# Optimization experiments

Hardware: AMD Instinct MI355X
Metric: run time of the kernel (lower is better)

## Reference

```python
import jax, jax.numpy as jnp
import numpy as np

N, E = 100000, 1600000
NFEAT, NHID, NCLASS = 128, 128, 40


def _glorot(key, shape):
    lim = float(np.sqrt(6.0 / (shape[0] + shape[1])))
    return jax.random.uniform(key, shape, jnp.float32, -lim, lim)


def setup_inputs() -> dict:
    key = jax.random.key(0)
    ks = jax.random.split(key, 9)
    x = jax.random.normal(ks[0], (N, NFEAT), jnp.float32)
    edge_index = jax.random.randint(ks[1], (2, E), 0, N, jnp.int32)
    return {
        "x": x,
        "edge_index": edge_index,
        # layer 1: lin_l (aggregated, with bias) and lin_r (root, no bias)
        "W1l": _glorot(ks[2], (NFEAT, NHID)), "b1": jnp.zeros((NHID,), jnp.float32),
        "W1r": _glorot(ks[3], (NFEAT, NHID)),
        "W2l": _glorot(ks[4], (NHID, NHID)), "b2": jnp.zeros((NHID,), jnp.float32),
        "W2r": _glorot(ks[5], (NHID, NHID)),
        "W3l": _glorot(ks[6], (NHID, NCLASS)), "b3": jnp.zeros((NCLASS,), jnp.float32),
        "W3r": _glorot(ks[7], (NHID, NCLASS)),
    }


def _sage_conv(x, src, dst, Wl, bl, Wr):
    # mean-aggregate source features at destination nodes (PyG SAGEConv, aggr='mean')
    msg = x[src]                                                  # [E, d] gather
    agg = jax.ops.segment_sum(msg, dst, num_segments=N)           # [N, d] scatter-add
    deg = jax.ops.segment_sum(jnp.ones((src.shape[0], 1), x.dtype), dst, num_segments=N)
    mean = agg / jnp.maximum(deg, 1.0)
    return mean @ Wl + bl + x @ Wr


def reference(x, edge_index, W1l, b1, W1r, W2l, b2, W2r, W3l, b3, W3r):
    src, dst = edge_index[0], edge_index[1]
    h = jax.nn.relu(_sage_conv(x, src, dst, W1l, b1, W1r))
    # dropout is identity in eval mode (training=False)
    h = jax.nn.relu(_sage_conv(h, src, dst, W2l, b2, W2r))
    embeddings = h
    logits = _sage_conv(h, src, dst, W3l, b3, W3r)
    return jax.nn.log_softmax(logits, axis=1), embeddings
```

## Files before the change

### kernel.cpp

```cpp
#include <hip/hip_runtime.h>
#include <math.h>

#define NCLASS 40
#define BEDG 1024
#define CAP 24576

typedef float f32x4 __attribute__((ext_vector_type(4)));
typedef __bf16 bf16x8 __attribute__((ext_vector_type(8)));

typedef __attribute__((address_space(1))) const void gv_t;
typedef __attribute__((address_space(3))) void lv_t;
#define GLOAD_LDS16(g, l) __builtin_amdgcn_global_load_lds((gv_t*)(g), (lv_t*)(l), 16, 0, 0)
#define NTL(p) __builtin_nontemporal_load(p)

__device__ inline unsigned short f2bf(float f) {
  unsigned u = __float_as_uint(f);
  unsigned r = (u + 0x7fff + ((u >> 16) & 1)) >> 16;
  return (unsigned short)r;
}
__device__ inline float bflo(unsigned v) { return __uint_as_float(v << 16); }
__device__ inline float bfhi(unsigned v) { return __uint_as_float(v & 0xffff0000u); }


__global__ void k_bcount(const int* __restrict__ dst, int E, int PART,
                         int* __restrict__ bcnt) {
  __shared__ int lc[8];
  int k = blockIdx.x;
  if (threadIdx.x < 8) lc[threadIdx.x] = 0;
  __syncthreads();
  int lo = k * BEDG, hi = min(lo + BEDG, E);
  for (int i = lo + threadIdx.x; i < hi; i += blockDim.x)
    atomicAdd(&lc[NTL(&dst[i]) / PART], 1);
  __syncthreads();
  if (threadIdx.x < 8) bcnt[k * 8 + threadIdx.x] = lc[threadIdx.x];
}

__global__ void k_bscanA(int* __restrict__ bcnt, int nbB, int* __restrict__ btot) {
  __shared__ int tmp[256];
  __shared__ int carryS;
  int b = blockIdx.x;
  int tid = threadIdx.x;
  if (tid == 0) carryS = 0;
  __syncthreads();
  for (int c0 = 0; c0 < nbB; c0 += 256) {
    int idx = c0 + tid;
    int v = (idx < nbB) ? bcnt[idx * 8 + b] : 0;
    tmp[tid] = v;
    __syncthreads();
    for (int d = 1; d < 256; d <<= 1) {
      int t = (tid >= d) ? tmp[tid - d] : 0;
      __syncthreads();
      tmp[tid] += t;
      __syncthreads();
    }
    if (idx < nbB) bcnt[idx * 8 + b] = carryS + tmp[tid] - v;
    __syncthreads();
    if (tid == 255) carryS += tmp[255];
    __syncthreads();
  }
  if (tid == 0) btot[b] = carryS;
}

__global__ void k_bbase(const int* __restrict__ btot, int* __restrict__ bbase) {
  if (threadIdx.x == 0) {
    int s = 0;
    for (int b = 0; b < 8; ++b) {
      bbase[b] = s;
      s += btot[b];
    }
    bbase[8] = s;
  }
}

__global__ void k_place(const int* __restrict__ dst, const int* __restrict__ src, int E,
                        int PART, const int* __restrict__ bcnt,
                        const int* __restrict__ bbase, int* __restrict__ ebuf) {
  __shared__ int lbase[8];
  __shared__ int lcnt[8];
  int k = blockIdx.x;
  if (threadIdx.x < 8) {
    lbase[threadIdx.x] = bbase[threadIdx.x] + bcnt[k * 8 + threadIdx.x];
    lcnt[threadIdx.x] = 0;
  }
  __syncthreads();
  int lo = k * BEDG, hi = min(lo + BEDG, E);
  for (int i = lo + threadIdx.x; i < hi; i += blockDim.x) {
    int d = NTL(&dst[i]);
    int s = NTL(&src[i]);
    int p = d / PART;
    int r = atomicAdd(&lcnt[p], 1);
    ebuf[lbase[p] + r] = (int)(((unsigned)(d - p * PART) << 17) | (unsigned)s);
  }
}

__global__ void k_bcount2(const int* __restrict__ ebuf, const int* __restrict__ bbase,
                          int CB, int* __restrict__ bcnt2) {
  __shared__ int lc[32];
  int p = blockIdx.x & 7, j = blockIdx.x >> 3;
  int tid = threadIdx.x;
  if (tid < 32) lc[tid] = 0;
  __syncthreads();
  int lo = bbase[p], hi = bbase[p + 1];
  for (int base = lo + j * BEDG; base < hi; base += CB * BEDG) {
    int end = min(base + BEDG, hi);
    for (int i = base + tid; i < end; i += 256)
      atomicAdd(&lc[(((unsigned)NTL(&ebuf[i])) >> 17) >> 9], 1);
  }
  __syncthreads();
  if (tid < 32) bcnt2[(p * CB + j) * 32 + tid] = lc[tid];
}

__global__ void k_bscan2(int* __restrict__ bcnt2, int CB, int* __restrict__ tot2) {
  __shared__ int tmp[256];
  int p = blockIdx.x >> 5, k = blockIdx.x & 31;
  int tid = threadIdx.x;
  int v = (tid < CB) ? bcnt2[(p * CB + tid) * 32 + k] : 0;
  tmp[tid] = v;
  __syncthreads();
  for (int d = 1; d < 256; d <<= 1) {
    int t = (tid >= d) ? tmp[tid - d] : 0;
    __syncthreads();
    tmp[tid] += t;
    __syncthreads();
  }
  if (tid < CB) bcnt2[(p * CB + tid) * 32 + k] = tmp[tid] - v;
  if (tid == 255) tot2[p * 32 + k] = tmp[255];
}

__global__ void k_base2(const int* __restrict__ bbase, const int* __restrict__ tot2,
                        int* __restrict__ base2) {
  int p = threadIdx.x;
  if (p >= 8) return;
  int s = bbase[p];
  for (int k = 0; k < 32; ++k) {
    base2[p * 32 + k] = s;
    s += tot2[p * 32 + k];
  }
}

__global__ void k_place2(const int* __restrict__ ebuf, const int* __restrict__ bbase,
                         const int* __restrict__ bcnt2, const int* __restrict__ base2,
                         int CB, int* __restrict__ ebuf2) {
  __shared__ int lb[32];
  int p = blockIdx.x & 7, j = blockIdx.x >> 3;
  int tid = threadIdx.x;
  if (tid < 32) lb[tid] = base2[p * 32 + tid] + bcnt2[(p * CB + j) * 32 + tid];
  __syncthreads();
  int lo = bbase[p], hi = bbase[p + 1];
  for (int base = lo + j * BEDG; base < hi; base += CB * BEDG) {
    int end = min(base + BEDG, hi);
    for (int i = base + tid; i < end; i += 256) {
      unsigned pk = (unsigned)NTL(&ebuf[i]);
      int pos = atomicAdd(&lb[(pk >> 17) >> 9], 1);
      ebuf2[pos] = (int)pk;
    }
  }
}

__global__ __launch_bounds__(256) void k_csr(const int* __restrict__ ebuf2,
                                             const int* __restrict__ base2,
                                             const int* __restrict__ tot2, int PART,
                                             int N, int E, int* __restrict__ off,
                                             int* __restrict__ col) {
  __shared__ int cnt[512];
  __shared__ int cur[512];
  __shared__ int tmp[256];
  __shared__ int stage[CAP];
  int p = blockIdx.x & 7, k = blockIdx.x >> 3;
  int tid = threadIdx.x;
  if (p == 0 && k == 0 && tid == 0) off[N] = E;
  int n0l = k << 9;
  if (n0l >= PART) return;
  int node0 = p * PART + n0l;
  if (node0 >= N) return;
  int nn = min(512, PART - n0l);
  nn = min(nn, N - node0);
  int lo = base2[p * 32 + k];
  int tot = tot2[p * 32 + k];

  cnt[tid] = 0;
  cnt[tid + 256] = 0;
  __syncthreads();
  for (int i = lo + tid; i < lo + tot; i += 256)
    atomicAdd(&cnt[(((unsigned)ebuf2[i]) >> 17) & 511], 1);
  __syncthreads();

  int v0 = cnt[2 * tid], v1 = cnt[2 * tid + 1];
  int s = v0 + v1;
  tmp[tid] = s;
  __syncthreads();
  for (int d = 1; d < 256; d <<= 1) {
    int t = (tid >= d) ? tmp[tid - d] : 0;
    __syncthreads();
    tmp[tid] += t;
    __syncthreads();
  }
  int excl = tmp[tid] - s;
  cnt[2 * tid] = excl;
  cnt[2 * tid + 1] = excl + v0;
  cur[2 * tid] = excl;
  cur[2 * tid + 1] = excl + v0;
  __syncthreads();

  for (int i = tid; i < nn; i += 256) off[node0 + i] = lo + cnt[i];

  if (tot <= CAP) {
    for (int i = lo + tid; i < lo + tot; i += 256) {
      unsigned pk = (unsigned)ebuf2[i];
      int pos = atomicAdd(&cur[(pk >> 17) & 511], 1);
      stage[pos] = (int)(pk & 0x1FFFFu);
    }
    __syncthreads();
    for (int i = tid; i < tot; i += 256) col[lo + i] = stage[i];
  } else {
    for (int i = lo + tid; i < lo + tot; i += 256) {
      unsigned pk = (unsigned)ebuf2[i];
      int pos = atomicAdd(&cur[(pk >> 17) & 511], 1);
      col[lo + pos] = (int)(pk & 0x1FFFFu);
    }
  }
}

__global__ void k_cast(const float4* __restrict__ x, uint4* __restrict__ xb, int n8) {
  int i = blockIdx.x * blockDim.x + threadIdx.x;
  if (i >= n8) return;
  float4 a = x[i * 2], b = x[i * 2 + 1];
  uint4 o;
  o.x = (unsigned)f2bf(a.x) | ((unsigned)f2bf(a.y) << 16);
  o.y = (unsigned)f2bf(a.z) | ((unsigned)f2bf(a.w) << 16);
  o.z = (unsigned)f2bf(b.x) | ((unsigned)f2bf(b.y) << 16);
  o.w = (unsigned)f2bf(b.z) | ((unsigned)f2bf(b.w) << 16);
  xb[i] = o;
}

__global__ void k_prepw(const float* __restrict__ W1l, const float* __restrict__ W1r,
                        const float* __restrict__ W2l, const float* __restrict__ W2r,
                        const float* __restrict__ W3l, const float* __restrict__ W3r,
                        unsigned short* __restrict__ Wth1, unsigned short* __restrict__ Wth2,
                        unsigned short* __restrict__ Wth3) {
  int idx = blockIdx.x * blockDim.x + threadIdx.x;
  if (idx < 32768) {
    int h = idx >> 14, c = (idx >> 7) & 127, k = idx & 127;
    const float* W = h ? W1r : W1l;
    Wth1[idx] = f2bf(W[k * 128 + c]);
  } else if (idx < 65536) {
    int j = idx - 32768;
    int h = j >> 14, c = (j >> 7) & 127, k = j & 127;
    const float* W = h ? W2r : W2l;
    Wth2[j] = f2bf(W[k * 128 + c]);
  } else if (idx < 65536 + 16384) {
    int j = idx - 65536;
    int h = j >> 13, c = (j >> 7) & 63, k = j & 127;
    float v = 0.f;
    if (c < NCLASS) v = (h ? W3r : W3l)[k * NCLASS + c];
    Wth3[j] = f2bf(v);
  }
}

#define ACC8(u, sc)                          \
  acc[0] = fmaf(bflo(u.x), sc, acc[0]);      \
  acc[1] = fmaf(bfhi(u.x), sc, acc[1]);      \
  acc[2] = fmaf(bflo(u.y), sc, acc[2]);      \
  acc[3] = fmaf(bfhi(u.y), sc, acc[3]);      \
  acc[4] = fmaf(bflo(u.z), sc, acc[4]);      \
  acc[5] = fmaf(bfhi(u.z), sc, acc[5]);      \
  acc[6] = fmaf(bflo(u.w), sc, acc[6]);      \
  acc[7] = fmaf(bfhi(u.w), sc, acc[7]);

__global__ void k_aggb(const char* __restrict__ X, const int* __restrict__ off,
                       const int* __restrict__ col, int n, uint4* __restrict__ out) {
  int wid = (blockIdx.x * blockDim.x + threadIdx.x) >> 6;
  int lane = threadIdx.x & 63;
  if (wid >= n) return;
  int g = lane >> 4, q = lane & 15;
  unsigned qb = (unsigned)q << 4;
  int s = off[wid], e = off[wid + 1];
  float acc[8];
#pragma unroll
  for (int t = 0; t < 8; ++t) acc[t] = 0.f;
  int e1 = e - 1;
  for (int j = s; j < e; j += 8) {
    int i0 = j + g, i1 = i0 + 4;
    int c0 = NTL(&col[min(i0, e1)]);
    int c1 = NTL(&col[min(i1, e1)]);
    float s0 = (i0 < e) ? 1.f : 0.f;
    float s1 = (i1 < e) ? 1.f : 0.f;
    uint4 u0 = *(const uint4*)(X + (((unsigned)c0 << 8) + qb));
    uint4 u1 = *(const uint4*)(X + (((unsigned)c1 << 8) + qb));
    ACC8(u0, s0);
    ACC8(u1, s1);
  }
#pragma unroll
  for (int t = 0; t < 8; ++t) {
    acc[t] += __shfl_xor(acc[t], 16);
    acc[t] += __shfl_xor(acc[t], 32);
  }
  float inv = 1.0f / fmaxf((float)(e - s), 1.0f);
  uint4 o;
  o.x = (unsigned)f2bf(acc[0] * inv) | ((unsigned)f2bf(acc[1] * inv) << 16);
  o.y = (unsigned)f2bf(acc[2] * inv) | ((unsigned)f2bf(acc[3] * inv) << 16);
  o.z = (unsigned)f2bf(acc[4] * inv) | ((unsigned)f2bf(acc[5] * inv) << 16);
  o.w = (unsigned)f2bf(acc[6] * inv) | ((unsigned)f2bf(acc[7] * inv) << 16);
  if (lane < 16) out[(size_t)wid * 16 + lane] = o;
}

template <int COLS, int HALVES, int EPI>
__global__ __launch_bounds__(256) void k_gemm_mfma(
    const unsigned short* __restrict__ Aagg, const unsigned short* __restrict__ Aroot,
    const unsigned short* __restrict__ Wth, const float* __restrict__ bias, int n,
    float* __restrict__ outF, unsigned short* __restrict__ outB) {
  constexpr int RF = 4;
  constexpr int CF = 4;
  __shared__ unsigned short aS[128 * 128];
  __shared__ unsigned short wS[COLS * 128];
  int tid = threadIdx.x;
  int w = tid >> 6, lane = tid & 63, l15 = lane & 15, kg = lane >> 4;
  int rowBase = blockIdx.x * 128;
  int r0 = (w >> 1) * 64;
  int c0 = (w & 1) * 64;

  f32x4 acc[RF][CF];
#pragma unroll
  for (int i = 0; i < RF; ++i)
#pragma unroll
    for (int j = 0; j < CF; ++j) acc[i][j] = (f32x4){0.f, 0.f, 0.f, 0.f};

#pragma unroll
  for (int half = 0; half < HALVES; ++half) {
    if (half) __syncthreads();
    {
      const unsigned short* As = half ? Aroot : Aagg;
#pragma unroll
      for (int it = 0; it < 8; ++it) {
        int row = it * 16 + (tid >> 4);
        int g = rowBase + row;
        g = (g < n) ? g : (n - 1);
        int cb = (tid & 15) << 4;
        int sb = cb ^ ((row & 7) << 4);
        const char* src = (const char*)(As + (size_t)g * 128) + sb;
        char* dst = (char*)aS + it * 4096 + (tid >> 6) * 1024;
        GLOAD_LDS16(src, dst);
      }
      const unsigned short* Ws = Wth + (size_t)half * COLS * 128;
#pragma unroll
      for (int it = 0; it < COLS / 16; ++it) {
        int c = it * 16 + (tid >> 4);
        int cb = (tid & 15) << 4;
        int sb = cb ^ ((c & 7) << 4);
        const char* src = (const char*)(Ws + (size_t)c * 128) + sb;
        char* dst = (char*)wS + it * 4096 + (tid >> 6) * 1024;
        GLOAD_LDS16(src, dst);
      }
      asm volatile("s_waitcnt vmcnt(0)" ::: "memory");
      __syncthreads();
    }
#pragma unroll
    for (int ks = 0; ks < 4; ++ks) {
      int kb = ks * 64 + kg * 16;
      bf16x8 av[RF], bv[CF];
#pragma unroll
      for (int i = 0; i < RF; ++i) {
        int row = r0 + i * 16 + l15;
        av[i] = *(const bf16x8*)((const char*)aS + row * 256 + (kb ^ ((row & 7) << 4)));
      }
#pragma unroll
      for (int j = 0; j < CF; ++j) {
        int c = c0 + j * 16 + l15;
        bv[j] = *(const bf16x8*)((const char*)wS + c * 256 + (kb ^ ((c & 7) << 4)));
      }
#pragma unroll
      for (int i = 0; i < RF; ++i)
#pragma unroll
        for (int j = 0; j < CF; ++j)
          acc[i][j] = __builtin_amdgcn_mfma_f32_16x16x32_bf16(av[i], bv[j], acc[i][j], 0, 0, 0);
    }
  }

  if (EPI == 3) {
    bool leftHalf = (c0 == 0);
    unsigned short* R3b = (unsigned short*)outF;
    float bcol[CF];
#pragma unroll
    for (int j = 0; j < CF; ++j) {
      int c = c0 + j * 16 + l15;
      bcol[j] = (!leftHalf && (c - 64) < NCLASS) ? bias[c - 64] : 0.f;
    }
#pragma unroll
    for (int i = 0; i < RF; ++i) {
#pragma unroll
      for (int r = 0; r < 4; ++r) {
        int row = rowBase + r0 + i * 16 + kg * 4 + r;
        if (row >= n) continue;
#pragma unroll
        for (int j = 0; j < CF; ++j) {
          int c = c0 + j * 16 + l15;
          if (leftHalf) {
            outB[(size_t)row * 64 + c] = f2bf(acc[i][j][r]);
          } else {
            R3b[(size_t)row * 64 + (c - 64)] = f2bf(acc[i][j][r] + bcol[j]);
          }
        }
      }
    }
  } else {
    float bcol[CF];
#pragma unroll
    for (int j = 0; j < CF; ++j) bcol[j] = bias[c0 + j * 16 + l15];
#pragma unroll
    for (int i = 0; i < RF; ++i) {
#pragma unroll
      for (int r = 0; r < 4; ++r) {
        int row = rowBase + r0 + i * 16 + kg * 4 + r;
        if (row >= n) continue;
#pragma unroll
        for (int j = 0; j < CF; ++j) {
          float v = fmaxf(acc[i][j][r] + bcol[j], 0.f);
          int c = c0 + j * 16 + l15;
          outB[(size_t)row * 128 + c] = f2bf(v);
          if (EPI == 1) outF[(size_t)row * 128 + c] = v;
        }
      }
    }
  }
}

__global__ void k_agg3ls(const char* __restrict__ Y3, const char* __restrict__ R3,
                         const int* __restrict__ off, const int* __restrict__ col, int n,
                         float* __restrict__ out) {
  int wid = (blockIdx.x * blockDim.x + threadIdx.x) >> 6;
  int lane = threadIdx.x & 63;
  if (wid >= n) return;
  int g = lane >> 3, q = lane & 7;
  unsigned qb = (unsigned)q << 4;
  int s = off[wid], e = off[wid + 1];
  float acc[8];
#pragma unroll
  for (int t = 0; t < 8; ++t) acc[t] = 0.f;
  int e1 = e - 1;
  for (int j = s; j < e; j += 16) {
    int i0 = j + g, i1 = i0 + 8;
    int c0 = NTL(&col[min(i0, e1)]);
    int c1 = NTL(&col[min(i1, e1)]);
    float s0 = (i0 < e) ? 1.f : 0.f;
    float s1 = (i1 < e) ? 1.f : 0.f;
    uint4 u0 = *(const uint4*)(Y3 + (((unsigned)c0 << 7) + qb));
    uint4 u1 = *(const uint4*)(Y3 + (((unsigned)c1 << 7) + qb));
    ACC8(u0, s0);
    ACC8(u1, s1);
  }
#pragma unroll
  for (int t = 0; t < 8; ++t) {
    acc[t] += __shfl_xor(acc[t], 8);
    acc[t] += __shfl_xor(acc[t], 16);
    acc[t] += __shfl_xor(acc[t], 32);
  }
  float inv = 1.0f / fmaxf((float)(e - s), 1.0f);
  uint4 ur = *(const uint4*)(R3 + (((unsigned)wid << 7) + qb));
  float v[8];
  v[0] = acc[0] * inv + bflo(ur.x);
  v[1] = acc[1] * inv + bfhi(ur.x);
  v[2] = acc[2] * inv + bflo(ur.y);
  v[3] = acc[3] * inv + bfhi(ur.y);
  v[4] = acc[4] * inv + bflo(ur.z);
  v[5] = acc[5] * inv + bfhi(ur.z);
  v[6] = acc[6] * inv + bflo(ur.w);
  v[7] = acc[7] * inv + bfhi(ur.w);
  bool valid = q < 5;
  float m = -INFINITY;
  if (valid) {
#pragma unroll
    for (int t = 0; t < 8; ++t) m = fmaxf(m, v[t]);
  }
  m = fmaxf(m, __shfl_xor(m, 1));
  m = fmaxf(m, __shfl_xor(m, 2));
  m = fmaxf(m, __shfl_xor(m, 4));
  float sum = 0.f;
  if (valid) {
#pragma unroll
    for (int t = 0; t < 8; ++t) sum += expf(v[t] - m);
  }
  sum += __shfl_xor(sum, 1);
  sum += __shfl_xor(sum, 2);
  sum += __shfl_xor(sum, 4);
  float ls = logf(sum);
  if (lane < 5) {
    float4 o0 = make_float4(v[0] - m - ls, v[1] - m - ls, v[2] - m - ls, v[3] - m - ls);
    float4 o1 = make_float4(v[4] - m - ls, v[5] - m - ls, v[6] - m - ls, v[7] - m - ls);
    float* op = out + (size_t)wid * NCLASS + lane * 8;
    *(float4*)op = o0;
    *(float4*)(op + 4) = o1;
  }
}

extern "C" void kernel_launch(void* const* d_in, const int* in_sizes, int n_in,
                              void* d_out, int out_size, void* d_ws, size_t ws_size,
                              hipStream_t stream) {
  const float* x = (const float*)d_in[0];
  const int* ei = (const int*)d_in[1];
  const float* W1l = (const float*)d_in[2];
  const float* b1 = (const float*)d_in[3];
  const float* W1r = (const float*)d_in[4];
  const float* W2l = (const float*)d_in[5];
  const float* b2 = (const float*)d_in[6];
  const float* W2r = (const float*)d_in[7];
  const float* W3l = (const float*)d_in[8];
  const float* b3 = (const float*)d_in[9];
  const float* W3r = (const float*)d_in[10];

  int N = in_sizes[0] / 128;
  int E = in_sizes[1] / 2;
  const int* src = ei;
  const int* dst = ei + E;
  int PART = (N + 7) / 8;
  int nbB = (E + BEDG - 1) / BEDG;
  int CB = (E + 8 * BEDG - 1) / (8 * BEDG);
  if (CB > 256) CB = 256;
  if (CB < 1) CB = 1;

  char* wptr = (char*)d_ws;
  auto alloc = [&](size_t bytes) {
    void* p = (void*)wptr;
    wptr += (bytes + 255) & ~(size_t)255;
    return p;
  };
  int* off = (int*)alloc((size_t)(N + 1) * 4);
  int* col = (int*)alloc((size_t)E * 4);
  int* bcnt = (int*)alloc((size_t)nbB * 8 * 4);
  int* btot = (int*)alloc(16 * 4);
  int* bbase = (int*)alloc(16 * 4);
  int* bcnt2 = (int*)alloc((size_t)8 * CB * 32 * 4);
  int* tot2 = (int*)alloc(256 * 4);
  int* base2 = (int*)alloc(256 * 4);
  unsigned short* Wth1 = (unsigned short*)alloc(32768 * 2);
  unsigned short* Wth2 = (unsigned short*)alloc(32768 * 2);
  unsigned short* Wth3 = (unsigned short*)alloc(16384 * 2);
  unsigned short* xb = (unsigned short*)alloc((size_t)N * 128 * 2);
  unsigned short* mb = (unsigned short*)alloc((size_t)N * 128 * 2);
  unsigned short* h1 = (unsigned short*)alloc((size_t)N * 128 * 2);
  unsigned short* h2 = (unsigned short*)alloc((size_t)N * 128 * 2);

  float* outLS = (float*)d_out;
  float* emb = (float*)d_out + (size_t)N * NCLASS;

  int* ebuf = (int*)h2;
  int* ebuf2 = (int*)h2 + E;
  unsigned short* Y3 = mb;
  unsigned short* R3b = h1;

  k_bcount<<<nbB, 256, 0, stream>>>(dst, E, PART, bcnt);
  k_bscanA<<<8, 256, 0, stream>>>(bcnt, nbB, btot);
  k_bbase<<<1, 64, 0, stream>>>(btot, bbase);
  k_place<<<nbB, 256, 0, stream>>>(dst, src, E, PART, bcnt, bbase, ebuf);
  k_bcount2<<<8 * CB, 256, 0, stream>>>(ebuf, bbase, CB, bcnt2);
  k_bscan2<<<256, 256, 0, stream>>>(bcnt2, CB, tot2);
  k_base2<<<1, 64, 0, stream>>>(bbase, tot2, base2);
  k_place2<<<8 * CB, 256, 0, stream>>>(ebuf, bbase, bcnt2, base2, CB, ebuf2);
  k_csr<<<256, 256, 0, stream>>>(ebuf2, base2, tot2, PART, N, E, off, col);

  int n8 = N * 16;
  k_cast<<<(n8 + 255) / 256, 256, 0, stream>>>((const float4*)x, (uint4*)xb, n8);
  k_prepw<<<(81920 + 255) / 256, 256, 0, stream>>>(W1l, W1r, W2l, W2r, W3l, W3r, Wth1,
                                                   Wth2, Wth3);

  int ab = (N * 64 + 255) / 256;
  int gb = (N + 127) / 128;

  k_aggb<<<ab, 256, 0, stream>>>((const char*)xb, off, col, N, (uint4*)mb);
  k_gemm_mfma<128, 2, 0><<<gb, 256, 0, stream>>>(mb, xb, Wth1, b1, N, nullptr, h1);
  k_aggb<<<ab, 256, 0, stream>>>((const char*)h1, off, col, N, (uint4*)mb);
  k_gemm_mfma<128, 2, 1><<<gb, 256, 0, stream>>>(mb, h1, Wth2, b2, N, emb, h2);
  k_gemm_mfma<128, 1, 3><<<gb, 256, 0, stream>>>(h2, nullptr, Wth3, b3, N, (float*)R3b, Y3);
  k_agg3ls<<<ab, 256, 0, stream>>>((const char*)Y3, (const char*)R3b, off, col, N, outLS);
}
```

Measured before the change: 313.9 us.

## Gather neighbor features in FP8 for all three mean aggregations

Adds FP8 (e4m3) copies of the input features, the layer-1 hidden state and the layer-3 projected logits. The edge-gather aggregation kernels now read these copies instead of the bf16 ones, halving the bytes fetched per neighbor row. Each lane decodes 16 values with packed FP8-to-FP32 conversions. The main cost being targeted is random gather bandwidth over 1.6M edges, paid for with extra FP8 writes in the cast and GEMM epilogues and a notable loss of precision that may fail tolerance.

```diff
diff --git a/kernel.cpp b/kernel.cpp
--- a/kernel.cpp
+++ b/kernel.cpp
@@ -6,6 +6,7 @@
 #define CAP 24576
 
 typedef float f32x4 __attribute__((ext_vector_type(4)));
+typedef float f32x2 __attribute__((ext_vector_type(2)));
 typedef __bf16 bf16x8 __attribute__((ext_vector_type(8)));
 
 typedef __attribute__((address_space(1))) const void gv_t;
@@ -20,7 +21,30 @@
 }
 __device__ inline float bflo(unsigned v) { return __uint_as_float(v << 16); }
 __device__ inline float bfhi(unsigned v) { return __uint_as_float(v & 0xffff0000u); }
-
+__device__ inline unsigned char f2fp8(float v) {
+  return (unsigned char)(__builtin_amdgcn_cvt_pk_fp8_f32(v, v, 0, false) & 0xff);
+}
+
+#define ACCQ(u, sc)                                                                  \
+  do {                                                                               \
+    f32x2 p_;                                                                        \
+    p_ = __builtin_amdgcn_cvt_pk_f32_fp8(u.x, false);                                \
+    acc[0] = fmaf(p_.x, sc, acc[0]); acc[1] = fmaf(p_.y, sc, acc[1]);                \
+    p_ = __builtin_amdgcn_cvt_pk_f32_fp8(u.x, true);                                 \
+    acc[2] = fmaf(p_.x, sc, acc[2]); acc[3] = fmaf(p_.y, sc, acc[3]);                \
+    p_ = __builtin_amdgcn_cvt_pk_f32_fp8(u.y, false);                                \
+    acc[4] = fmaf(p_.x, sc, acc[4]); acc[5] = fmaf(p_.y, sc, acc[5]);                \
+    p_ = __builtin_amdgcn_cvt_pk_f32_fp8(u.y, true);                                 \
+    acc[6] = fmaf(p_.x, sc, acc[6]); acc[7] = fmaf(p_.y, sc, acc[7]);                \
+    p_ = __builtin_amdgcn_cvt_pk_f32_fp8(u.z, false);                                \
+    acc[8] = fmaf(p_.x, sc, acc[8]); acc[9] = fmaf(p_.y, sc, acc[9]);                \
+    p_ = __builtin_amdgcn_cvt_pk_f32_fp8(u.z, true);                                 \
+    acc[10] = fmaf(p_.x, sc, acc[10]); acc[11] = fmaf(p_.y, sc, acc[11]);            \
+    p_ = __builtin_amdgcn_cvt_pk_f32_fp8(u.w, false);                                \
+    acc[12] = fmaf(p_.x, sc, acc[12]); acc[13] = fmaf(p_.y, sc, acc[13]);            \
+    p_ = __builtin_amdgcn_cvt_pk_f32_fp8(u.w, true);                                 \
+    acc[14] = fmaf(p_.x, sc, acc[14]); acc[15] = fmaf(p_.y, sc, acc[15]);            \
+  } while (0)
 
 __global__ void k_bcount(const int* __restrict__ dst, int E, int PART,
                          int* __restrict__ bcnt) {
@@ -221,7 +245,8 @@
   }
 }
 
-__global__ void k_cast(const float4* __restrict__ x, uint4* __restrict__ xb, int n8) {
+__global__ void k_cast(const float4* __restrict__ x, uint4* __restrict__ xb,
+                       uint2* __restrict__ xq, int n8) {
   int i = blockIdx.x * blockDim.x + threadIdx.x;
   if (i >= n8) return;
   float4 a = x[i * 2], b = x[i * 2 + 1];
@@ -231,6 +256,11 @@
   o.z = (unsigned)f2bf(b.x) | ((unsigned)f2bf(b.y) << 16);
   o.w = (unsigned)f2bf(b.z) | ((unsigned)f2bf(b.w) << 16);
   xb[i] = o;
+  unsigned lo = __builtin_amdgcn_cvt_pk_fp8_f32(a.x, a.y, 0, false);
+  lo = __builtin_amdgcn_cvt_pk_fp8_f32(a.z, a.w, lo, true);
+  unsigned hi = __builtin_amdgcn_cvt_pk_fp8_f32(b.x, b.y, 0, false);
+  hi = __builtin_amdgcn_cvt_pk_fp8_f32(b.z, b.w, hi, true);
+  xq[i] = make_uint2(lo, hi);
 }
 
 __global__ void k_prepw(const float* __restrict__ W1l, const float* __restrict__ W1r,
@@ -257,51 +287,49 @@
   }
 }
 
-#define ACC8(u, sc)                          \
-  acc[0] = fmaf(bflo(u.x), sc, acc[0]);      \
-  acc[1] = fmaf(bfhi(u.x), sc, acc[1]);      \
-  acc[2] = fmaf(bflo(u.y), sc, acc[2]);      \
-  acc[3] = fmaf(bfhi(u.y), sc, acc[3]);      \
-  acc[4] = fmaf(bflo(u.z), sc, acc[4]);      \
-  acc[5] = fmaf(bfhi(u.z), sc, acc[5]);      \
-  acc[6] = fmaf(bflo(u.w), sc, acc[6]);      \
-  acc[7] = fmaf(bfhi(u.w), sc, acc[7]);
-
-__global__ void k_aggb(const char* __restrict__ X, const int* __restrict__ off,
+__global__ void k_aggq(const char* __restrict__ Xq, const int* __restrict__ off,
                        const int* __restrict__ col, int n, uint4* __restrict__ out) {
   int wid = (blockIdx.x * blockDim.x + threadIdx.x) >> 6;
   int lane = threadIdx.x & 63;
   if (wid >= n) return;
-  int g = lane >> 4, q = lane & 15;
+  int g = lane >> 3, q = lane & 7;
   unsigned qb = (unsigned)q << 4;
   int s = off[wid], e = off[wid + 1];
-  float acc[8];
-#pragma unroll
-  for (int t = 0; t < 8; ++t) acc[t] = 0.f;
+  float acc[16];
+#pragma unroll
+  for (int t = 0; t < 16; ++t) acc[t] = 0.f;
   int e1 = e - 1;
-  for (int j = s; j < e; j += 8) {
-    int i0 = j + g, i1 = i0 + 4;
+  for (int j = s; j < e; j += 16) {
+    int i0 = j + g, i1 = i0 + 8;
     int c0 = NTL(&col[min(i0, e1)]);
     int c1 = NTL(&col[min(i1, e1)]);
     float s0 = (i0 < e) ? 1.f : 0.f;
     float s1 = (i1 < e) ? 1.f : 0.f;
-    uint4 u0 = *(const uint4*)(X + (((unsigned)c0 << 8) + qb));
-    uint4 u1 = *(const uint4*)(X + (((unsigned)c1 << 8) + qb));
-    ACC8(u0, s0);
-    ACC8(u1, s1);
-  }
-#pragma unroll
-  for (int t = 0; t < 8; ++t) {
+    uint4 u0 = *(const uint4*)(Xq + (((unsigned)c0 << 7) + qb));
+    uint4 u1 = *(const uint4*)(Xq + (((unsigned)c1 << 7) + qb));
+    ACCQ(u0, s0);
+    ACCQ(u1, s1);
+  }
+#pragma unroll
+  for (int t = 0; t < 16; ++t) {
+    acc[t] += __shfl_xor(acc[t], 8);
     acc[t] += __shfl_xor(acc[t], 16);
     acc[t] += __shfl_xor(acc[t], 32);
   }
   float inv = 1.0f / fmaxf((float)(e - s), 1.0f);
-  uint4 o;
-  o.x = (unsigned)f2bf(acc[0] * inv) | ((unsigned)f2bf(acc[1] * inv) << 16);
-  o.y = (unsigned)f2bf(acc[2] * inv) | ((unsigned)f2bf(acc[3] * inv) << 16);
-  o.z = (unsigned)f2bf(acc[4] * inv) | ((unsigned)f2bf(acc[5] * inv) << 16);
-  o.w = (unsigned)f2bf(acc[6] * inv) | ((unsigned)f2bf(acc[7] * inv) << 16);
-  if (lane < 16) out[(size_t)wid * 16 + lane] = o;
+  if (lane < 8) {
+    uint4 o0, o1;
+    o0.x = (unsigned)f2bf(acc[0] * inv) | ((unsigned)f2bf(acc[1] * inv) << 16);
+    o0.y = (unsigned)f2bf(acc[2] * inv) | ((unsigned)f2bf(acc[3] * inv) << 16);
+    o0.z = (unsigned)f2bf(acc[4] * inv) | ((unsigned)f2bf(acc[5] * inv) << 16);
+    o0.w = (unsigned)f2bf(acc[6] * inv) | ((unsigned)f2bf(acc[7] * inv) << 16);
+    o1.x = (unsigned)f2bf(acc[8] * inv) | ((unsigned)f2bf(acc[9] * inv) << 16);
+    o1.y = (unsigned)f2bf(acc[10] * inv) | ((unsigned)f2bf(acc[11] * inv) << 16);
+    o1.z = (unsigned)f2bf(acc[12] * inv) | ((unsigned)f2bf(acc[13] * inv) << 16);
+    o1.w = (unsigned)f2bf(acc[14] * inv) | ((unsigned)f2bf(acc[15] * inv) << 16);
+    out[(size_t)wid * 16 + q * 2] = o0;
+    out[(size_t)wid * 16 + q * 2 + 1] = o1;
+  }
 }
 
 template <int COLS, int HALVES, int EPI>
@@ -378,6 +406,7 @@
 
   if (EPI == 3) {
     bool leftHalf = (c0 == 0);
+    unsigned char* Y3q = (unsigned char*)outB;
     unsigned short* R3b = (unsigned short*)outF;
     float bcol[CF];
 #pragma unroll
@@ -395,7 +424,7 @@
         for (int j = 0; j < CF; ++j) {
           int c = c0 + j * 16 + l15;
           if (leftHalf) {
-            outB[(size_t)row * 64 + c] = f2bf(acc[i][j][r]);
+            Y3q[(size_t)row * 64 + c] = f2fp8(acc[i][j][r]);
           } else {
             R3b[(size_t)row * 64 + (c - 64)] = f2bf(acc[i][j][r] + bcol[j]);
           }
@@ -418,77 +447,84 @@
           int c = c0 + j * 16 + l15;
           outB[(size_t)row * 128 + c] = f2bf(v);
           if (EPI == 1) outF[(size_t)row * 128 + c] = v;
+          if (EPI == 0) ((unsigned char*)outF)[(size_t)row * 128 + c] = f2fp8(v);
         }
       }
     }
   }
 }
 
-__global__ void k_agg3ls(const char* __restrict__ Y3, const char* __restrict__ R3,
-                         const int* __restrict__ off, const int* __restrict__ col, int n,
-                         float* __restrict__ out) {
+__global__ void k_agg3q(const char* __restrict__ Y3q, const char* __restrict__ R3,
+                        const int* __restrict__ off, const int* __restrict__ col, int n,
+                        float* __restrict__ out) {
   int wid = (blockIdx.x * blockDim.x + threadIdx.x) >> 6;
   int lane = threadIdx.x & 63;
   if (wid >= n) return;
-  int g = lane >> 3, q = lane & 7;
+  int g = lane >> 2, q = lane & 3;
   unsigned qb = (unsigned)q << 4;
   int s = off[wid], e = off[wid + 1];
-  float acc[8];
-#pragma unroll
-  for (int t = 0; t < 8; ++t) acc[t] = 0.f;
+  float acc[16];
+#pragma unroll
+  for (int t = 0; t < 16; ++t) acc[t] = 0.f;
   int e1 = e - 1;
   for (int j = s; j < e; j += 16) {
-    int i0 = j + g, i1 = i0 + 8;
+    int i0 = j + g;
     int c0 = NTL(&col[min(i0, e1)]);
-    int c1 = NTL(&col[min(i1, e1)]);
     float s0 = (i0 < e) ? 1.f : 0.f;
-    float s1 = (i1 < e) ? 1.f : 0.f;
-    uint4 u0 = *(const uint4*)(Y3 + (((unsigned)c0 << 7) + qb));
-    uint4 u1 = *(const uint4*)(Y3 + (((unsigned)c1 << 7) + qb));
-    ACC8(u0, s0);
-    ACC8(u1, s1);
-  }
-#pragma unroll
-  for (int t = 0; t < 8; ++t) {
+    uint4 u0 = *(const uint4*)(Y3q + (((unsigned)c0 << 6) + qb));
+    ACCQ(u0, s0);
+  }
+#pragma unroll
+  for (int t = 0; t < 16; ++t) {
+    acc[t] += __shfl_xor(acc[t], 4);
     acc[t] += __shfl_xor(acc[t], 8);
     acc[t] += __shfl_xor(acc[t], 16);
     acc[t] += __shfl_xor(acc[t], 32);
   }
   float inv = 1.0f / fmaxf((float)(e - s), 1.0f);
-  uint4 ur = *(const uint4*)(R3 + (((unsigned)wid << 7) + qb));
-  float v[8];
-  v[0] = acc[0] * inv + bflo(ur.x);
-  v[1] = acc[1] * inv + bfhi(ur.x);
-  v[2] = acc[2] * inv + bflo(ur.y);
-  v[3] = acc[3] * inv + bfhi(ur.y);
-  v[4] = acc[4] * inv + bflo(ur.z);
-  v[5] = acc[5] * inv + bfhi(ur.z);
-  v[6] = acc[6] * inv + bflo(ur.w);
-  v[7] = acc[7] * inv + bfhi(ur.w);
-  bool valid = q < 5;
+  uint4 ur0 = *(const uint4*)(R3 + (((unsigned)wid << 7) + ((unsigned)q << 5)));
+  uint4 ur1 = *(const uint4*)(R3 + (((unsigned)wid << 7) + ((unsigned)q << 5) + 16));
+  float v[16];
+  v[0] = fmaf(acc[0], inv, bflo(ur0.x));
+  v[1] = fmaf(acc[1], inv, bfhi(ur0.x));
+  v[2] = fmaf(acc[2], inv, bflo(ur0.y));
+  v[3] = fmaf(acc[3], inv, bfhi(ur0.y));
+  v[4] = fmaf(acc[4], inv, bflo(ur0.z));
+  v[5] = fmaf(acc[5], inv, bfhi(ur0.z));
+  v[6] = fmaf(acc[6], inv, bflo(ur0.w));
+  v[7] = fmaf(acc[7], inv, bfhi(ur0.w));
+  v[8] = fmaf(acc[8], inv, bflo(ur1.x));
+  v[9] = fmaf(acc[9], inv, bfhi(ur1.x));
+  v[10] = fmaf(acc[10], inv, bflo(ur1.y));
+  v[11] = fmaf(acc[11], inv, bfhi(ur1.y));
+  v[12] = fmaf(acc[12], inv, bflo(ur1.z));
+  v[13] = fmaf(acc[13], inv, bfhi(ur1.z));
+  v[14] = fmaf(acc[14], inv, bflo(ur1.w));
+  v[15] = fmaf(acc[15], inv, bfhi(ur1.w));
+  int nv = (q < 2) ? 16 : ((q == 2) ? 8 : 0);
   float m = -INFINITY;
-  if (valid) {
-#pragma unroll
-    for (int t = 0; t < 8; ++t) m = fmaxf(m, v[t]);
-  }
+#pragma unroll
+  for (int t = 0; t < 16; ++t)
+    if (t < nv) m = fmaxf(m, v[t]);
   m = fmaxf(m, __shfl_xor(m, 1));
   m = fmaxf(m, __shfl_xor(m, 2));
-  m = fmaxf(m, __shfl_xor(m, 4));
   float sum = 0.f;
-  if (valid) {
-#pragma unroll
-    for (int t = 0; t < 8; ++t) sum += expf(v[t] - m);
-  }
+#pragma unroll
+  for (int t = 0; t < 16; ++t)
+    if (t < nv) sum += expf(v[t] - m);
   sum += __shfl_xor(sum, 1);
   sum += __shfl_xor(sum, 2);
-  sum += __shfl_xor(sum, 4);
   float ls = logf(sum);
-  if (lane < 5) {
-    float4 o0 = make_float4(v[0] - m - ls, v[1] - m - ls, v[2] - m - ls, v[3] - m - ls);
-    float4 o1 = make_float4(v[4] - m - ls, v[5] - m - ls, v[6] - m - ls, v[7] - m - ls);
-    float* op = out + (size_t)wid * NCLASS + lane * 8;
-    *(float4*)op = o0;
-    *(float4*)(op + 4) = o1;
+  if (g == 0 && nv > 0) {
+    float* op = out + (size_t)wid * NCLASS + q * 16;
+#pragma unroll
+    for (int t = 0; t < 16; t += 4) {
+      if (t < nv) {
+        float4 o = make_float4(v[t] - m - ls, v[t + 1] - m - ls, v[t + 2] - m - ls,
+                               v[t + 3] - m - ls);
+        *(float4*)(op + t) = o;
+      }
+    }
   }
 }
 
@@ -538,13 +574,15 @@
   unsigned short* mb = (unsigned short*)alloc((size_t)N * 128 * 2);
   unsigned short* h1 = (unsigned short*)alloc((size_t)N * 128 * 2);
   unsigned short* h2 = (unsigned short*)alloc((size_t)N * 128 * 2);
+  unsigned char* xq = (unsigned char*)alloc((size_t)N * 128);
+  unsigned char* h1q = (unsigned char*)alloc((size_t)N * 128);
 
   float* outLS = (float*)d_out;
   float* emb = (float*)d_out + (size_t)N * NCLASS;
 
   int* ebuf = (int*)h2;
   int* ebuf2 = (int*)h2 + E;
-  unsigned short* Y3 = mb;
+  unsigned char* Y3q = (unsigned char*)mb;
   unsigned short* R3b = h1;
 
   k_bcount<<<nbB, 256, 0, stream>>>(dst, E, PART, bcnt);
@@ -558,17 +596,19 @@
   k_csr<<<256, 256, 0, stream>>>(ebuf2, base2, tot2, PART, N, E, off, col);
 
   int n8 = N * 16;
-  k_cast<<<(n8 + 255) / 256, 256, 0, stream>>>((const float4*)x, (uint4*)xb, n8);
+  k_cast<<<(n8 + 255) / 256, 256, 0, stream>>>((const float4*)x, (uint4*)xb, (uint2*)xq,
+                                               n8);
   k_prepw<<<(81920 + 255) / 256, 256, 0, stream>>>(W1l, W1r, W2l, W2r, W3l, W3r, Wth1,
                                                    Wth2, Wth3);
 
   int ab = (N * 64 + 255) / 256;
   int gb = (N + 127) / 128;
 
-  k_aggb<<<ab, 256, 0, stream>>>((const char*)xb, off, col, N, (uint4*)mb);
-  k_gemm_mfma<128, 2, 0><<<gb, 256, 0, stream>>>(mb, xb, Wth1, b1, N, nullptr, h1);
-  k_aggb<<<ab, 256, 0, stream>>>((const char*)h1, off, col, N, (uint4*)mb);
+  k_aggq<<<ab, 256, 0, stream>>>((const char*)xq, off, col, N, (uint4*)mb);
+  k_gemm_mfma<128, 2, 0><<<gb, 256, 0, stream>>>(mb, xb, Wth1, b1, N, (float*)h1q, h1);
+  k_aggq<<<ab, 256, 0, stream>>>((const char*)h1q, off, col, N, (uint4*)mb);
   k_gemm_mfma<128, 2, 1><<<gb, 256, 0, stream>>>(mb, h1, Wth2, b2, N, emb, h2);
-  k_gemm_mfma<128, 1, 3><<<gb, 256, 0, stream>>>(h2, nullptr, Wth3, b3, N, (float*)R3b, Y3);
-  k_agg3ls<<<ab, 256, 0, stream>>>((const char*)Y3, (const char*)R3b, off, col, N, outLS);
-}
+  k_gemm_mfma<128, 1, 3><<<gb, 256, 0, stream>>>(h2, nullptr, Wth3, b3, N, (float*)R3b,
+                                                 (unsigned short*)Y3q);
+  k_agg3q<<<ab, 256, 0, stream>>>((const char*)Y3q, (const char*)R3b, off, col, N, outLS);
+}
```

Result: slower. 335.7 us (+6.9%).
